# Optimization experiments

Hardware: AMD Instinct MI355X
Metric: run time of the kernel (lower is better)

The kernel has to match this reference:

```python
import jax, jax.numpy as jnp
import numpy as np

N = 100000      # nodes
E = 1600000     # edges (before self-loops)
IN_DIM = 128
HEADS = 4
C = 32          # hid_dim // heads = 128 // 4
SLOPE = 0.2     # PyG GATConv default negative_slope


def setup_inputs() -> dict:
    key = jax.random.key(0)
    k1, k2, k3, k4, k5 = jax.random.split(key, 5)
    x = jax.random.normal(k1, (N, IN_DIM), dtype=jnp.float32)
    edge_index = jax.random.randint(k2, (2, E), 0, N, dtype=jnp.int32)
    # learned parameters of GATConv
    W = jax.random.normal(k3, (IN_DIM, HEADS * C), dtype=jnp.float32) / np.sqrt(IN_DIM)
    att_src = jax.random.normal(k4, (HEADS, C), dtype=jnp.float32) * 0.1
    att_dst = jax.random.normal(k5, (HEADS, C), dtype=jnp.float32) * 0.1
    bias = jnp.zeros((HEADS * C,), dtype=jnp.float32)
    return {"x": x, "edge_index": edge_index, "W": W,
            "att_src": att_src, "att_dst": att_dst, "bias": bias}


def reference(x, edge_index, W, att_src, att_dst, bias):
    # PyG GATConv default add_self_loops=True
    loops = jnp.arange(N, dtype=edge_index.dtype)
    ei = jnp.concatenate([edge_index, jnp.stack([loops, loops])], axis=1)
    src, dst = ei[0], ei[1]                       # messages flow src -> dst

    h = (x @ W).reshape(N, HEADS, C)              # [N,H,C]
    a_src = jnp.einsum('nhc,hc->nh', h, att_src)  # [N,H]
    a_dst = jnp.einsum('nhc,hc->nh', h, att_dst)  # [N,H]

    e = a_src[src] + a_dst[dst]                   # [E+N,H] per-edge logits
    e = jax.nn.leaky_relu(e, SLOPE)

    # segment softmax over edges sharing a destination node
    m = jax.ops.segment_max(e, dst, num_segments=N)        # [N,H]
    e = jnp.exp(e - m[dst])
    s = jax.ops.segment_sum(e, dst, num_segments=N)        # [N,H]
    alpha = e / (s[dst] + 1e-16)                            # [E+N,H]

    msg = h[src] * alpha[:, :, None]                        # [E+N,H,C]
    out = jax.ops.segment_sum(msg, dst, num_segments=N)     # [N,H,C]
    return out.reshape(N, HEADS * C) + bias                 # concat heads + bias
```

## Files before the change

kernel.cpp:

```cpp
#include <hip/hip_runtime.h>
#include <cstddef>

#define HEADS 4
#define HC 128
#define SLOPE 0.2f
#define NPBUCK 256
#define NSBMAX 512
#define SBCAP 5120
#define CHUNK 4096
#define GTILE 128

using half8 = __attribute__((ext_vector_type(8))) _Float16;
using f32x4 = __attribute__((ext_vector_type(4))) float;

__device__ __forceinline__ float edge_w(float v) {
    v = v > 0.f ? v : SLOPE * v;
    return __expf(v);
}
__device__ __forceinline__ float2 up2(unsigned w) {
    union { unsigned u; _Float16 f[2]; } c; c.u = w;
    return make_float2((float)c.f[0], (float)c.f[1]);
}

__global__ void wt_kernel(const float* __restrict__ W,
                          const float* __restrict__ att_src,
                          const float* __restrict__ att_dst,
                          _Float16* __restrict__ WTh,
                          _Float16* __restrict__ WAttT) {
    int k = threadIdx.x;
    int nn = blockIdx.x;
    WTh[nn * HC + k] = (_Float16)W[k * HC + nn];
    if (nn == 0) {
#pragma unroll
        for (int head = 0; head < 4; ++head) {
            float s = 0.f, d = 0.f;
#pragma unroll
            for (int c = 0; c < 32; ++c) {
                float w = W[k * HC + head * 32 + c];
                s += w * att_src[head * 32 + c];
                d += w * att_dst[head * 32 + c];
            }
            WAttT[head * HC + k]       = (_Float16)s;
            WAttT[(4 + head) * HC + k] = (_Float16)d;
        }
#pragma unroll
        for (int r = 8; r < 16; ++r) WAttT[r * HC + k] = (_Float16)0.f;
    }
}

__global__ __launch_bounds__(256)
void gemm_att_count_kernel(const float* __restrict__ x, const _Float16* __restrict__ WTh,
                           const _Float16* __restrict__ WAttT,
                           _Float16* __restrict__ h2,
                           float* __restrict__ a_s, float* __restrict__ a_d,
                           const int* __restrict__ ei, int* __restrict__ cnt2d,
                           int gb, int E, int n) {
    __shared__ _Float16 lA[GTILE * HC];
    __shared__ _Float16 lB[HC * HC];
    __shared__ _Float16 lAtt[16 * HC];
    int tid = threadIdx.x;

    if (blockIdx.x >= gb) {
        int* cnt = (int*)lA;
        int cb = blockIdx.x - gb;
        for (int i = tid; i < NSBMAX; i += 256) cnt[i] = 0;
        __syncthreads();
        int Etot = E + n;
        int e0 = cb * CHUNK;
        int eend = e0 + CHUNK; if (eend > Etot) eend = Etot;
        for (int e = e0 + tid; e < eend; e += 256) {
            int dst = (e < E) ? ei[E + e] : (e - E);
            atomicAdd(&cnt[dst >> 8], 1);
        }
        __syncthreads();
        int* row = cnt2d + (size_t)cb * NSBMAX;
        for (int i = tid; i < NSBMAX; i += 256) row[i] = cnt[i];
        return;
    }

    int r0 = blockIdx.x * GTILE;
#pragma unroll
    for (int it = 0; it < 16; ++it) {
        int idx = it * 256 + tid;
        int r   = idx >> 5;
        int c8  = idx & 31;
        int rowg = r0 + r; if (rowg >= n) rowg = n - 1;
        float4 f = *(const float4*)(x + (size_t)rowg * HC + c8 * 4);
        union { _Float16 h[4]; uint2 u; } pk;
        pk.h[0] = (_Float16)f.x; pk.h[1] = (_Float16)f.y;
        pk.h[2] = (_Float16)f.z; pk.h[3] = (_Float16)f.w;
        int byte = r * 256 + (((c8 >> 1) ^ (r & 15)) << 4) + ((c8 & 1) << 3);
        *(uint2*)((char*)lA + byte) = pk.u;
    }
#pragma unroll
    for (int it = 0; it < 8; ++it) {
        int idx = it * 256 + tid;
        int r = idx >> 4, c = idx & 15;
        uint4 v = *(const uint4*)(WTh + (size_t)r * HC + c * 8);
        *(uint4*)((char*)lB + r * 256 + ((c ^ (r & 15)) << 4)) = v;
    }
    {
        int r = tid >> 4, c = tid & 15;
        uint4 v = *(const uint4*)(WAttT + (size_t)r * HC + c * 8);
        *(uint4*)((char*)lAtt + r * 256 + ((c ^ r) << 4)) = v;
    }
    __syncthreads();

    int wv   = tid >> 6;
    int lane = tid & 63;
    int t    = lane & 15;
    int q    = lane >> 4;

    f32x4 acc[2][8];
    f32x4 accA[2];
#pragma unroll
    for (int rt = 0; rt < 2; ++rt) {
        accA[rt] = (f32x4){0.f, 0.f, 0.f, 0.f};
#pragma unroll
        for (int ct = 0; ct < 8; ++ct) acc[rt][ct] = (f32x4){0.f, 0.f, 0.f, 0.f};
    }

    int ar0 = wv * 32 + t;
    int ar1 = ar0 + 16;
#pragma unroll
    for (int kc = 0; kc < 4; ++kc) {
        int c = kc * 4 + q;
        half8 a0 = *(const half8*)((char*)lA + ar0 * 256 + ((c ^ t) << 4));
        half8 a1 = *(const half8*)((char*)lA + ar1 * 256 + ((c ^ t) << 4));
#pragma unroll
        for (int ct = 0; ct < 8; ++ct) {
            int rb = ct * 16 + t;
            half8 b = *(const half8*)((char*)lB + rb * 256 + ((c ^ t) << 4));
            acc[0][ct] = __builtin_amdgcn_mfma_f32_16x16x32_f16(a0, b, acc[0][ct], 0, 0, 0);
            acc[1][ct] = __builtin_amdgcn_mfma_f32_16x16x32_f16(a1, b, acc[1][ct], 0, 0, 0);
        }
        half8 bA = *(const half8*)((char*)lAtt + t * 256 + ((c ^ t) << 4));
        accA[0] = __builtin_amdgcn_mfma_f32_16x16x32_f16(a0, bA, accA[0], 0, 0, 0);
        accA[1] = __builtin_amdgcn_mfma_f32_16x16x32_f16(a1, bA, accA[1], 0, 0, 0);
    }

#pragma unroll
    for (int rt = 0; rt < 2; ++rt) {
        int Rbase = r0 + wv * 32 + rt * 16;
#pragma unroll
        for (int reg = 0; reg < 4; ++reg) {
            int row = Rbase + q * 4 + reg;
            if (row < n) {
#pragma unroll
                for (int ct = 0; ct < 8; ++ct)
                    h2[(size_t)row * HC + ct * 16 + t] = (_Float16)acc[rt][ct][reg];
            }
        }
#pragma unroll
        for (int reg = 0; reg < 4; ++reg) {
            int row = Rbase + q * 4 + reg;
            if (row < n && t < 8) {
                if (t < 4) a_s[(size_t)row * 4 + t]       = accA[rt][reg];
                else       a_d[(size_t)row * 4 + (t - 4)] = accA[rt][reg];
            }
        }
    }
}

__global__ __launch_bounds__(512)
void colscan_kernel(const int* __restrict__ cnt2d, int* __restrict__ base2d,
                    int* __restrict__ bucketend, int nchunks) {
    __shared__ int tmp[512];
    int b = blockIdx.x;
    int t = threadIdx.x;
    int v = (t < nchunks) ? cnt2d[(size_t)t * NSBMAX + b] : 0;
    tmp[t] = v;
    __syncthreads();
#pragma unroll
    for (int off = 1; off < 512; off <<= 1) {
        int u = (t >= off) ? tmp[t - off] : 0;
        __syncthreads();
        tmp[t] += u;
        __syncthreads();
    }
    if (t < nchunks) base2d[(size_t)t * NSBMAX + b] = b * SBCAP + tmp[t] - v;
    if (t == 511) bucketend[b] = b * SBCAP + tmp[511];
}

__global__ __launch_bounds__(256)
void scatter_kernel(const int* __restrict__ ei, int E, int n,
                    const int* __restrict__ base2d, int* __restrict__ binned) {
    __shared__ int cnt[NSBMAX];
    __shared__ int lstart[NSBMAX];
    __shared__ int pos[256];
    __shared__ int gbase[NSBMAX];
    __shared__ int valA[CHUNK];
    __shared__ unsigned short bkA[CHUNK];
    int tid = threadIdx.x;
    int Etot = E + n;
    int e0 = blockIdx.x * CHUNK;
    int eend = e0 + CHUNK; if (eend > Etot) eend = Etot;
    int tot = eend - e0;

    const int* brow = base2d + (size_t)blockIdx.x * NSBMAX;
    for (int i = tid; i < NSBMAX; i += 256) { cnt[i] = 0; gbase[i] = brow[i]; }
    __syncthreads();

    int esv[CHUNK / 256]; int edv[CHUNK / 256];
#pragma unroll
    for (int it = 0; it < CHUNK / 256; ++it) {
        int e = e0 + it * 256 + tid;
        int src = 0, dst = 0;
        if (e < Etot) {
            if (e < E) { src = ei[e]; dst = ei[E + e]; }
            else       { src = e - E; dst = src; }
            atomicAdd(&cnt[dst >> 8], 1);
        }
        esv[it] = src; edv[it] = dst;
    }
    __syncthreads();

    int c0 = cnt[2 * tid], c1 = cnt[2 * tid + 1];
    int p = c0 + c1;
    pos[tid] = p;
    __syncthreads();
#pragma unroll
    for (int off = 1; off < 256; off <<= 1) {
        int v = (tid >= off) ? pos[tid - off] : 0;
        __syncthreads();
        pos[tid] += v;
        __syncthreads();
    }
    int excl = pos[tid] - p;
    lstart[2 * tid]     = excl;
    lstart[2 * tid + 1] = excl + c0;
    __syncthreads();

    for (int i = tid; i < NSBMAX; i += 256) cnt[i] = lstart[i];
    __syncthreads();
#pragma unroll
    for (int it = 0; it < CHUNK / 256; ++it) {
        int e = e0 + it * 256 + tid;
        if (e < Etot) {
            int bk = edv[it] >> 8;
            int lp = atomicAdd(&cnt[bk], 1);
            valA[lp] = esv[it] | ((edv[it] & 255) << 17);
            bkA[lp] = (unsigned short)bk;
        }
    }
    __syncthreads();

    for (int j = tid; j < tot; j += 256) {
        int b = bkA[j];
        binned[gbase[b] + (j - lstart[b])] = valA[j];
    }
}

__global__ __launch_bounds__(256)
void place_kernel(const int* __restrict__ bucketend, const int* __restrict__ binned,
                  int* __restrict__ sorted, int* __restrict__ rowstart,
                  int* __restrict__ deg, int n) {
    __shared__ int win[SBCAP];
    __shared__ int cnt[256];
    __shared__ int pos[256];
    int b = blockIdx.x;
    int dst0 = b << 8;
    int rows = n - dst0; if (rows > 256) rows = 256;
    int tid = threadIdx.x;
    int wstart = b * SBCAP;
    int tot = bucketend[b] - wstart;

    cnt[tid] = 0;
    for (int j = tid; j < tot; j += 256) win[j] = binned[wstart + j];
    __syncthreads();
    for (int j = tid; j < tot; j += 256)
        atomicAdd(&cnt[win[j] >> 17], 1);
    __syncthreads();

    int d = cnt[tid];
    pos[tid] = d;
    __syncthreads();
#pragma unroll
    for (int off = 1; off < 256; off <<= 1) {
        int v = (tid >= off) ? pos[tid - off] : 0;
        __syncthreads();
        pos[tid] += v;
        __syncthreads();
    }
    int excl = pos[tid] - d;
    if (tid < rows) {
        rowstart[dst0 + tid] = wstart + excl;
        deg[dst0 + tid] = d;
    }
    cnt[tid] = excl;
    __syncthreads();
    for (int j = tid; j < tot; j += 256) {
        int v = win[j];
        int p = atomicAdd(&cnt[v >> 17], 1);
        sorted[wstart + p] = v & 0x1FFFF;
    }
}

__global__ __launch_bounds__(256)
void agg_kernel(const int* __restrict__ rowstart, const int* __restrict__ deg,
                const int* __restrict__ sorted,
                const float* __restrict__ a_s, const float* __restrict__ a_d,
                const _Float16* __restrict__ h2, const float* __restrict__ bias,
                float* __restrict__ out, int n) {
    int dst = blockIdx.x * 4 + (threadIdx.x >> 6);
    if (dst >= n) return;
    int lane = threadIdx.x & 63;
    int li   = lane & 15;
    int sub  = lane >> 4;
    int head = li >> 2;
    int start = rowstart[dst];
    int cntv  = deg[dst];

    float ad = a_d[(size_t)dst * 4 + head];
    const uint4* h4 = (const uint4*)h2;
    float acc[8] = {0.f,0.f,0.f,0.f,0.f,0.f,0.f,0.f};
    float wsum = 0.f;

    for (int j = 0; j < cntv; j += 16) {
        int   sv[4]; float wv[4]; uint4 hv[4];
#pragma unroll
        for (int k = 0; k < 4; ++k) {
            int idx = j + k * 4 + sub;
            bool valid = idx < cntv;
            sv[k] = sorted[start + (valid ? idx : cntv - 1)];
            wv[k] = valid ? 1.f : 0.f;
        }
#pragma unroll
        for (int k = 0; k < 4; ++k)
            hv[k] = h4[(size_t)sv[k] * 16 + li];
#pragma unroll
        for (int k = 0; k < 4; ++k) {
            float w = wv[k] * edge_w(a_s[(size_t)sv[k] * 4 + head] + ad);
            float2 f0 = up2(hv[k].x), f1 = up2(hv[k].y),
                   f2 = up2(hv[k].z), f3 = up2(hv[k].w);
            acc[0] = fmaf(w, f0.x, acc[0]); acc[1] = fmaf(w, f0.y, acc[1]);
            acc[2] = fmaf(w, f1.x, acc[2]); acc[3] = fmaf(w, f1.y, acc[3]);
            acc[4] = fmaf(w, f2.x, acc[4]); acc[5] = fmaf(w, f2.y, acc[5]);
            acc[6] = fmaf(w, f3.x, acc[6]); acc[7] = fmaf(w, f3.y, acc[7]);
            wsum += w;
        }
    }

#pragma unroll
    for (int k = 0; k < 8; ++k) {
        acc[k] += __shfl_xor(acc[k], 16);
        acc[k] += __shfl_xor(acc[k], 32);
    }
    wsum += __shfl_xor(wsum, 16);
    wsum += __shfl_xor(wsum, 32);

    if (sub == 0) {
        float inv = 1.f / wsum;
        float4 b0 = ((const float4*)bias)[li * 2];
        float4 b1 = ((const float4*)bias)[li * 2 + 1];
        float4 o0 = make_float4(acc[0]*inv + b0.x, acc[1]*inv + b0.y,
                                acc[2]*inv + b0.z, acc[3]*inv + b0.w);
        float4 o1 = make_float4(acc[4]*inv + b1.x, acc[5]*inv + b1.y,
                                acc[6]*inv + b1.z, acc[7]*inv + b1.w);
        float4* op = (float4*)(out + (size_t)dst * HC);
        op[li * 2]     = o0;
        op[li * 2 + 1] = o1;
    }
}

extern "C" void kernel_launch(void* const* d_in, const int* in_sizes, int n_in,
                              void* d_out, int out_size, void* d_ws, size_t ws_size,
                              hipStream_t stream) {
    const float* x       = (const float*)d_in[0];
    const int*   ei      = (const int*)d_in[1];
    const float* W       = (const float*)d_in[2];
    const float* att_src = (const float*)d_in[3];
    const float* att_dst = (const float*)d_in[4];
    const float* bias    = (const float*)d_in[5];

    int n = in_sizes[0] / HC;
    int E = in_sizes[1] / 2;
    int Etot = E + n;
    int nbuck   = (n + NPBUCK - 1) / NPBUCK;
    int nchunks = (Etot + CHUNK - 1) / CHUNK;
    int gb      = (n + GTILE - 1) / GTILE;

    _Float16* h2     = (_Float16*)d_ws;
    _Float16* WTh    = h2 + (size_t)n * HC;
    _Float16* WAttT  = WTh + HC * HC;
    float* a_s       = (float*)(WAttT + 16 * HC);
    float* a_d       = a_s + (size_t)n * HEADS;
    int*   cnt2d     = (int*)(a_d + (size_t)n * HEADS);
    int*   base2d    = cnt2d + (size_t)nchunks * NSBMAX;
    int*   bucketend = base2d + (size_t)nchunks * NSBMAX;
    int*   rowstart  = bucketend + NSBMAX;
    int*   deg       = rowstart + n;
    int*   binned    = deg + n;
    int*   sorted    = binned + (size_t)nbuck * SBCAP;
    float* out       = (float*)d_out;

    wt_kernel<<<HC, HC, 0, stream>>>(W, att_src, att_dst, WTh, WAttT);
    gemm_att_count_kernel<<<gb + nchunks, 256, 0, stream>>>(
        x, WTh, WAttT, h2, a_s, a_d, ei, cnt2d, gb, E, n);
    colscan_kernel<<<nbuck, 512, 0, stream>>>(cnt2d, base2d, bucketend, nchunks);
    scatter_kernel<<<nchunks, 256, 0, stream>>>(ei, E, n, base2d, binned);
    place_kernel<<<nbuck, 256, 0, stream>>>(bucketend, binned, sorted,
                                            rowstart, deg, n);
    agg_kernel<<<(n + 3) / 4, 256, 0, stream>>>(rowstart, deg, sorted,
                                                a_s, a_d, h2, bias, out, n);
}
```

Baseline: 236.3 us.

## Split count from GEMM kernel, halve GEMM tile, fuse place load with histogram

The fused GEMM+count kernel becomes two launches. The count kernel no longer carries the GEMM's large LDS footprint, and the GEMM tile drops from 128 to 64 rows, so each wave holds one 16-row MFMA tile. This cuts LDS and registers per block and should raise occupancy and block count. In place_kernel, loading the window and the histogram atomics now happen in a single pass. The costs are an extra kernel launch, serialising count before the GEMM, and each block reloading W for fewer rows.

```diff
diff --git a/kernel.cpp b/kernel.cpp
--- a/kernel.cpp
+++ b/kernel.cpp
@@ -8,7 +8,7 @@
 #define NSBMAX 512
 #define SBCAP 5120
 #define CHUNK 4096
-#define GTILE 128
+#define GTILE 64
 
 using half8 = __attribute__((ext_vector_type(8))) _Float16;
 using f32x4 = __attribute__((ext_vector_type(4))) float;
@@ -49,38 +49,38 @@
 }
 
 __global__ __launch_bounds__(256)
-void gemm_att_count_kernel(const float* __restrict__ x, const _Float16* __restrict__ WTh,
-                           const _Float16* __restrict__ WAttT,
-                           _Float16* __restrict__ h2,
-                           float* __restrict__ a_s, float* __restrict__ a_d,
-                           const int* __restrict__ ei, int* __restrict__ cnt2d,
-                           int gb, int E, int n) {
+void count_kernel(const int* __restrict__ ei, int E, int n,
+                  int* __restrict__ cnt2d) {
+    __shared__ int cnt[NSBMAX];
+    int tid = threadIdx.x;
+    int cb = blockIdx.x;
+    for (int i = tid; i < NSBMAX; i += 256) cnt[i] = 0;
+    __syncthreads();
+    int Etot = E + n;
+    int e0 = cb * CHUNK;
+    int eend = e0 + CHUNK; if (eend > Etot) eend = Etot;
+    for (int e = e0 + tid; e < eend; e += 256) {
+        int dst = (e < E) ? ei[E + e] : (e - E);
+        atomicAdd(&cnt[dst >> 8], 1);
+    }
+    __syncthreads();
+    int* row = cnt2d + (size_t)cb * NSBMAX;
+    for (int i = tid; i < NSBMAX; i += 256) row[i] = cnt[i];
+}
+
+__global__ __launch_bounds__(256)
+void gemm_att_kernel(const float* __restrict__ x, const _Float16* __restrict__ WTh,
+                     const _Float16* __restrict__ WAttT,
+                     _Float16* __restrict__ h2,
+                     float* __restrict__ a_s, float* __restrict__ a_d, int n) {
     __shared__ _Float16 lA[GTILE * HC];
     __shared__ _Float16 lB[HC * HC];
     __shared__ _Float16 lAtt[16 * HC];
     int tid = threadIdx.x;
 
-    if (blockIdx.x >= gb) {
-        int* cnt = (int*)lA;
-        int cb = blockIdx.x - gb;
-        for (int i = tid; i < NSBMAX; i += 256) cnt[i] = 0;
-        __syncthreads();
-        int Etot = E + n;
-        int e0 = cb * CHUNK;
-        int eend = e0 + CHUNK; if (eend > Etot) eend = Etot;
-        for (int e = e0 + tid; e < eend; e += 256) {
-            int dst = (e < E) ? ei[E + e] : (e - E);
-            atomicAdd(&cnt[dst >> 8], 1);
-        }
-        __syncthreads();
-        int* row = cnt2d + (size_t)cb * NSBMAX;
-        for (int i = tid; i < NSBMAX; i += 256) row[i] = cnt[i];
-        return;
-    }
-
     int r0 = blockIdx.x * GTILE;
 #pragma unroll
-    for (int it = 0; it < 16; ++it) {
+    for (int it = 0; it < 8; ++it) {
         int idx = it * 256 + tid;
         int r   = idx >> 5;
         int c8  = idx & 31;
@@ -111,53 +111,42 @@
     int t    = lane & 15;
     int q    = lane >> 4;
 
-    f32x4 acc[2][8];
-    f32x4 accA[2];
-#pragma unroll
-    for (int rt = 0; rt < 2; ++rt) {
-        accA[rt] = (f32x4){0.f, 0.f, 0.f, 0.f};
-#pragma unroll
-        for (int ct = 0; ct < 8; ++ct) acc[rt][ct] = (f32x4){0.f, 0.f, 0.f, 0.f};
-    }
-
-    int ar0 = wv * 32 + t;
-    int ar1 = ar0 + 16;
+    f32x4 acc[8];
+    f32x4 accA = (f32x4){0.f, 0.f, 0.f, 0.f};
+#pragma unroll
+    for (int ct = 0; ct < 8; ++ct) acc[ct] = (f32x4){0.f, 0.f, 0.f, 0.f};
+
+    int ar = wv * 16 + t;
 #pragma unroll
     for (int kc = 0; kc < 4; ++kc) {
         int c = kc * 4 + q;
-        half8 a0 = *(const half8*)((char*)lA + ar0 * 256 + ((c ^ t) << 4));
-        half8 a1 = *(const half8*)((char*)lA + ar1 * 256 + ((c ^ t) << 4));
+        half8 a0 = *(const half8*)((char*)lA + ar * 256 + ((c ^ t) << 4));
 #pragma unroll
         for (int ct = 0; ct < 8; ++ct) {
             int rb = ct * 16 + t;
             half8 b = *(const half8*)((char*)lB + rb * 256 + ((c ^ t) << 4));
-            acc[0][ct] = __builtin_amdgcn_mfma_f32_16x16x32_f16(a0, b, acc[0][ct], 0, 0, 0);
-            acc[1][ct] = __builtin_amdgcn_mfma_f32_16x16x32_f16(a1, b, acc[1][ct], 0, 0, 0);
+            acc[ct] = __builtin_amdgcn_mfma_f32_16x16x32_f16(a0, b, acc[ct], 0, 0, 0);
         }
         half8 bA = *(const half8*)((char*)lAtt + t * 256 + ((c ^ t) << 4));
-        accA[0] = __builtin_amdgcn_mfma_f32_16x16x32_f16(a0, bA, accA[0], 0, 0, 0);
-        accA[1] = __builtin_amdgcn_mfma_f32_16x16x32_f16(a1, bA, accA[1], 0, 0, 0);
-    }
-
-#pragma unroll
-    for (int rt = 0; rt < 2; ++rt) {
-        int Rbase = r0 + wv * 32 + rt * 16;
-#pragma unroll
-        for (int reg = 0; reg < 4; ++reg) {
-            int row = Rbase + q * 4 + reg;
-            if (row < n) {
-#pragma unroll
-                for (int ct = 0; ct < 8; ++ct)
-                    h2[(size_t)row * HC + ct * 16 + t] = (_Float16)acc[rt][ct][reg];
-            }
-        }
-#pragma unroll
-        for (int reg = 0; reg < 4; ++reg) {
-            int row = Rbase + q * 4 + reg;
-            if (row < n && t < 8) {
-                if (t < 4) a_s[(size_t)row * 4 + t]       = accA[rt][reg];
-                else       a_d[(size_t)row * 4 + (t - 4)] = accA[rt][reg];
-            }
+        accA = __builtin_amdgcn_mfma_f32_16x16x32_f16(a0, bA, accA, 0, 0, 0);
+    }
+
+    int Rbase = r0 + wv * 16;
+#pragma unroll
+    for (int reg = 0; reg < 4; ++reg) {
+        int row = Rbase + q * 4 + reg;
+        if (row < n) {
+#pragma unroll
+            for (int ct = 0; ct < 8; ++ct)
+                h2[(size_t)row * HC + ct * 16 + t] = (_Float16)acc[ct][reg];
+        }
+    }
+#pragma unroll
+    for (int reg = 0; reg < 4; ++reg) {
+        int row = Rbase + q * 4 + reg;
+        if (row < n && t < 8) {
+            if (t < 4) a_s[(size_t)row * 4 + t]       = accA[reg];
+            else       a_d[(size_t)row * 4 + (t - 4)] = accA[reg];
         }
     }
 }
@@ -266,10 +255,12 @@
     int tot = bucketend[b] - wstart;
 
     cnt[tid] = 0;
-    for (int j = tid; j < tot; j += 256) win[j] = binned[wstart + j];
-    __syncthreads();
-    for (int j = tid; j < tot; j += 256)
-        atomicAdd(&cnt[win[j] >> 17], 1);
+    __syncthreads();
+    for (int j = tid; j < tot; j += 256) {
+        int v = binned[wstart + j];
+        win[j] = v;
+        atomicAdd(&cnt[v >> 17], 1);
+    }
     __syncthreads();
 
     int d = cnt[tid];
@@ -395,8 +386,8 @@
     float* out       = (float*)d_out;
 
     wt_kernel<<<HC, HC, 0, stream>>>(W, att_src, att_dst, WTh, WAttT);
-    gemm_att_count_kernel<<<gb + nchunks, 256, 0, stream>>>(
-        x, WTh, WAttT, h2, a_s, a_d, ei, cnt2d, gb, E, n);
+    count_kernel<<<nchunks, 256, 0, stream>>>(ei, E, n, cnt2d);
+    gemm_att_kernel<<<gb, 256, 0, stream>>>(x, WTh, WAttT, h2, a_s, a_d, n);
     colscan_kernel<<<nbuck, 512, 0, stream>>>(cnt2d, base2d, bucketend, nchunks);
     scatter_kernel<<<nchunks, 256, 0, stream>>>(ei, E, n, base2d, binned);
     place_kernel<<<nbuck, 256, 0, stream>>>(bucketend, binned, sorted,
```

Measured after the change: 239.6 us. No clear change (+1.4%).

## Replace count pass and column scan with global atomic bucket cursors

Applied to the files above, without the earlier changes.

Drops the per-chunk bucket counting inside the GEMM launch and the column-scan kernel. Each scatter block now reserves space in each bucket with one global atomicAdd on a per-bucket cursor, which wt_kernel initialises. After scatter the cursor holds the bucket end for place_kernel. This removes one kernel launch and one full read of the destination indices, at the cost of global atomic contention and a bucket order inside each window that depends on block scheduling. place_kernel also merges its load and histogram loops into one.

```diff
diff --git a/kernel.cpp b/kernel.cpp
--- a/kernel.cpp
+++ b/kernel.cpp
@@ -26,10 +26,15 @@
                           const float* __restrict__ att_src,
                           const float* __restrict__ att_dst,
                           _Float16* __restrict__ WTh,
-                          _Float16* __restrict__ WAttT) {
+                          _Float16* __restrict__ WAttT,
+                          int* __restrict__ cursor) {
     int k = threadIdx.x;
     int nn = blockIdx.x;
     WTh[nn * HC + k] = (_Float16)W[k * HC + nn];
+    if (nn < 4) {
+        int b = nn * 128 + k;
+        cursor[b] = b * SBCAP;
+    }
     if (nn == 0) {
 #pragma unroll
         for (int head = 0; head < 4; ++head) {
@@ -49,34 +54,14 @@
 }
 
 __global__ __launch_bounds__(256)
-void gemm_att_count_kernel(const float* __restrict__ x, const _Float16* __restrict__ WTh,
-                           const _Float16* __restrict__ WAttT,
-                           _Float16* __restrict__ h2,
-                           float* __restrict__ a_s, float* __restrict__ a_d,
-                           const int* __restrict__ ei, int* __restrict__ cnt2d,
-                           int gb, int E, int n) {
+void gemm_att_kernel(const float* __restrict__ x, const _Float16* __restrict__ WTh,
+                     const _Float16* __restrict__ WAttT,
+                     _Float16* __restrict__ h2,
+                     float* __restrict__ a_s, float* __restrict__ a_d, int n) {
     __shared__ _Float16 lA[GTILE * HC];
     __shared__ _Float16 lB[HC * HC];
     __shared__ _Float16 lAtt[16 * HC];
     int tid = threadIdx.x;
-
-    if (blockIdx.x >= gb) {
-        int* cnt = (int*)lA;
-        int cb = blockIdx.x - gb;
-        for (int i = tid; i < NSBMAX; i += 256) cnt[i] = 0;
-        __syncthreads();
-        int Etot = E + n;
-        int e0 = cb * CHUNK;
-        int eend = e0 + CHUNK; if (eend > Etot) eend = Etot;
-        for (int e = e0 + tid; e < eend; e += 256) {
-            int dst = (e < E) ? ei[E + e] : (e - E);
-            atomicAdd(&cnt[dst >> 8], 1);
-        }
-        __syncthreads();
-        int* row = cnt2d + (size_t)cb * NSBMAX;
-        for (int i = tid; i < NSBMAX; i += 256) row[i] = cnt[i];
-        return;
-    }
 
     int r0 = blockIdx.x * GTILE;
 #pragma unroll
@@ -162,29 +147,9 @@
     }
 }
 
-__global__ __launch_bounds__(512)
-void colscan_kernel(const int* __restrict__ cnt2d, int* __restrict__ base2d,
-                    int* __restrict__ bucketend, int nchunks) {
-    __shared__ int tmp[512];
-    int b = blockIdx.x;
-    int t = threadIdx.x;
-    int v = (t < nchunks) ? cnt2d[(size_t)t * NSBMAX + b] : 0;
-    tmp[t] = v;
-    __syncthreads();
-#pragma unroll
-    for (int off = 1; off < 512; off <<= 1) {
-        int u = (t >= off) ? tmp[t - off] : 0;
-        __syncthreads();
-        tmp[t] += u;
-        __syncthreads();
-    }
-    if (t < nchunks) base2d[(size_t)t * NSBMAX + b] = b * SBCAP + tmp[t] - v;
-    if (t == 511) bucketend[b] = b * SBCAP + tmp[511];
-}
-
 __global__ __launch_bounds__(256)
 void scatter_kernel(const int* __restrict__ ei, int E, int n,
-                    const int* __restrict__ base2d, int* __restrict__ binned) {
+                    int* __restrict__ cursor, int* __restrict__ binned) {
     __shared__ int cnt[NSBMAX];
     __shared__ int lstart[NSBMAX];
     __shared__ int pos[256];
@@ -197,8 +162,7 @@
     int eend = e0 + CHUNK; if (eend > Etot) eend = Etot;
     int tot = eend - e0;
 
-    const int* brow = base2d + (size_t)blockIdx.x * NSBMAX;
-    for (int i = tid; i < NSBMAX; i += 256) { cnt[i] = 0; gbase[i] = brow[i]; }
+    for (int i = tid; i < NSBMAX; i += 256) cnt[i] = 0;
     __syncthreads();
 
     int esv[CHUNK / 256]; int edv[CHUNK / 256];
@@ -214,6 +178,11 @@
         esv[it] = src; edv[it] = dst;
     }
     __syncthreads();
+
+    for (int i = tid; i < NSBMAX; i += 256) {
+        int c = cnt[i];
+        gbase[i] = (c > 0) ? atomicAdd(&cursor[i], c) : 0;
+    }
 
     int c0 = cnt[2 * tid], c1 = cnt[2 * tid + 1];
     int p = c0 + c1;
@@ -266,10 +235,12 @@
     int tot = bucketend[b] - wstart;
 
     cnt[tid] = 0;
-    for (int j = tid; j < tot; j += 256) win[j] = binned[wstart + j];
-    __syncthreads();
-    for (int j = tid; j < tot; j += 256)
-        atomicAdd(&cnt[win[j] >> 17], 1);
+    __syncthreads();
+    for (int j = tid; j < tot; j += 256) {
+        int v = binned[wstart + j];
+        win[j] = v;
+        atomicAdd(&cnt[v >> 17], 1);
+    }
     __syncthreads();
 
     int d = cnt[tid];
@@ -385,21 +356,17 @@
     _Float16* WAttT  = WTh + HC * HC;
     float* a_s       = (float*)(WAttT + 16 * HC);
     float* a_d       = a_s + (size_t)n * HEADS;
-    int*   cnt2d     = (int*)(a_d + (size_t)n * HEADS);
-    int*   base2d    = cnt2d + (size_t)nchunks * NSBMAX;
-    int*   bucketend = base2d + (size_t)nchunks * NSBMAX;
-    int*   rowstart  = bucketend + NSBMAX;
+    int*   cursor    = (int*)(a_d + (size_t)n * HEADS);
+    int*   rowstart  = cursor + NSBMAX;
     int*   deg       = rowstart + n;
     int*   binned    = deg + n;
     int*   sorted    = binned + (size_t)nbuck * SBCAP;
     float* out       = (float*)d_out;
 
-    wt_kernel<<<HC, HC, 0, stream>>>(W, att_src, att_dst, WTh, WAttT);
-    gemm_att_count_kernel<<<gb + nchunks, 256, 0, stream>>>(
-        x, WTh, WAttT, h2, a_s, a_d, ei, cnt2d, gb, E, n);
-    colscan_kernel<<<nbuck, 512, 0, stream>>>(cnt2d, base2d, bucketend, nchunks);
-    scatter_kernel<<<nchunks, 256, 0, stream>>>(ei, E, n, base2d, binned);
-    place_kernel<<<nbuck, 256, 0, stream>>>(bucketend, binned, sorted,
+    wt_kernel<<<HC, HC, 0, stream>>>(W, att_src, att_dst, WTh, WAttT, cursor);
+    gemm_att_kernel<<<gb, 256, 0, stream>>>(x, WTh, WAttT, h2, a_s, a_d, n);
+    scatter_kernel<<<nchunks, 256, 0, stream>>>(ei, E, n, cursor, binned);
+    place_kernel<<<nbuck, 256, 0, stream>>>(cursor, binned, sorted,
                                             rowstart, deg, n);
     agg_kernel<<<(n + 3) / 4, 256, 0, stream>>>(rowstart, deg, sorted,
                                                 a_s, a_d, h2, bias, out, n);
```

Measured after the change: 230.6 us. 2.4% less time.
